# Performance work log

Hardware: AMD Instinct MI355X
Metric: run time of the kernel (lower is better)

Reference implementation:

```python
import jax, jax.numpy as jnp
import numpy as np

N = 50000      # nodes
E = 800000     # edges (avg degree 16)
D_IN, D_H, D_OUT = 128, 128, 64


def setup_inputs() -> dict:
    key = jax.random.key(0)
    ks = jax.random.split(key, 12)
    s = 0.05  # weight init scale
    return {
        "x": jax.random.normal(ks[0], (N, D_IN), jnp.float32),
        "edge_index": jax.random.randint(ks[1], (2, E), 0, N, dtype=jnp.int64),
        "Wl0": jax.random.normal(ks[2], (D_H, D_IN), jnp.float32) * s,
        "bl0": jax.random.normal(ks[3], (D_H,), jnp.float32) * s,
        "Wr0": jax.random.normal(ks[4], (D_H, D_IN), jnp.float32) * s,
        "Wl1": jax.random.normal(ks[5], (D_H, D_H), jnp.float32) * s,
        "bl1": jax.random.normal(ks[6], (D_H,), jnp.float32) * s,
        "Wr1": jax.random.normal(ks[7], (D_H, D_H), jnp.float32) * s,
        "Wl2": jax.random.normal(ks[8], (D_OUT, D_H), jnp.float32) * s,
        "bl2": jax.random.normal(ks[9], (D_OUT,), jnp.float32) * s,
        "Wr2": jax.random.normal(ks[10], (D_OUT, D_H), jnp.float32) * s,
    }


def _sage_layer(h, src, dst, Wl, bl, Wr):
    # mean aggregation over incoming neighbors: out[i] = mean_{j in N(i)} h[j]
    n = h.shape[0]
    agg = jax.ops.segment_sum(h[src], dst, num_segments=n)          # [N, D]
    deg = jax.ops.segment_sum(jnp.ones((src.shape[0],), h.dtype), dst,
                              num_segments=n)                        # [N]
    mean = agg / jnp.maximum(deg, 1.0)[:, None]  # empty rows -> 0, matches torch_sparse
    # lin_l(agg) + lin_r(self); lin_r has no bias in PyG SAGEConv
    return mean @ Wl.T + bl + h @ Wr.T


def reference(x, edge_index, Wl0, bl0, Wr0, Wl1, bl1, Wr1, Wl2, bl2, Wr2):
    src, dst = edge_index[1], edge_index[0]  # adj row = dst, col = src
    h = jax.nn.relu(_sage_layer(x, src, dst, Wl0, bl0, Wr0))
    h = jax.nn.relu(_sage_layer(h, src, dst, Wl1, bl1, Wr1))
    h = _sage_layer(h, src, dst, Wl2, bl2, Wr2)
    return jax.nn.log_softmax(h, axis=1)
```

## Files before the change

kernel.cpp:

```cpp
#include <hip/hip_runtime.h>
#include <hip/hip_bf16.h>


typedef __attribute__((ext_vector_type(8))) short bf16x8;
typedef __attribute__((ext_vector_type(4))) float f32x4;

#define NPB 128
#define BCAP 2560
#define EPB 8192
#define EPT 32
#define CPAD 16

__device__ __forceinline__ unsigned short f2bf(float f) {
    unsigned int u = __builtin_bit_cast(unsigned int, f);
    u += 0x7fffu + ((u >> 16) & 1u);
    return (unsigned short)(u >> 16);
}
__device__ __forceinline__ float bf2f(unsigned int bits16) {
    return __builtin_bit_cast(float, bits16 << 16);
}


__global__ __launch_bounds__(256) void distribute_kernel(const int* __restrict__ dst,
                                                         const int* __restrict__ srcv,
                                                         int* __restrict__ gcnt,
                                                         unsigned int* __restrict__ staging,
                                                         int E, int NBc) {
    __shared__ unsigned int stage[EPB];
    __shared__ int hist[400];
    __shared__ int lstart[400];
    __shared__ int gbase[400];
    __shared__ int scanbuf[256];
    int t = threadIdx.x;
    int e0 = blockIdx.x * EPB;
    unsigned int w[EPT];

    for (int b = t; b < NBc + 1; b += 256) hist[b] = 0;
    __syncthreads();

#pragma unroll
    for (int i = 0; i < EPT; ++i) {
        int e = e0 + i * 256 + t;
        unsigned int word = 0xFFFFFFFFu;
        if (e < E) word = ((unsigned int)dst[e] << 16) | (unsigned int)srcv[e];
        w[i] = word;
        int b = (int)(word >> 23); if (b > NBc) b = NBc;
        atomicAdd(&hist[b], 1);
    }
    __syncthreads();

    int b0 = 2 * t, b1 = 2 * t + 1;
    int h0 = (b0 <= NBc) ? hist[b0] : 0;
    int h1 = (b1 <= NBc) ? hist[b1] : 0;
    int pair = h0 + h1;
    scanbuf[t] = pair;
    __syncthreads();
    for (int off = 1; off < 256; off <<= 1) {
        int v = (t >= off) ? scanbuf[t - off] : 0;
        __syncthreads();
        scanbuf[t] += v;
        __syncthreads();
    }
    int excl = scanbuf[t] - pair;
    if (b0 <= NBc) lstart[b0] = excl;
    if (b1 <= NBc) lstart[b1] = excl + h0;
    __syncthreads();

    for (int b = t; b < NBc; b += 256) {
        int h = hist[b];
        gbase[b] = h ? atomicAdd(&gcnt[b * CPAD], h) : 0;
    }
    for (int b = t; b < NBc + 1; b += 256) hist[b] = lstart[b];
    __syncthreads();

#pragma unroll
    for (int i = 0; i < EPT; ++i) {
        unsigned int word = w[i];
        int b = (int)(word >> 23); if (b > NBc) b = NBc;
        int p = atomicAdd(&hist[b], 1);
        stage[p] = word;
    }
    __syncthreads();

    int total = lstart[NBc];
    for (int i = t; i < total; i += 256) {
        unsigned int word = stage[i];
        int b = (int)(word >> 23);
        int gpos = gbase[b] + (i - lstart[b]);
        staging[(size_t)b * BCAP + gpos] = word;
    }
}


__global__ __launch_bounds__(512) void bucket_scan_kernel(const int* __restrict__ gcnt,
                                                          int* __restrict__ base, int NBc,
                                                          int* __restrict__ rowptr_last) {
    __shared__ int sh[512];
    int t = threadIdx.x;
    int v = (t < NBc) ? gcnt[t * CPAD] : 0;
    sh[t] = v; __syncthreads();
    for (int off = 1; off < 512; off <<= 1) {
        int u = (t >= off) ? sh[t - off] : 0;
        __syncthreads();
        sh[t] += u;
        __syncthreads();
    }
    if (t < NBc) base[t] = sh[t] - v;
    if (t == 511) *rowptr_last = sh[511];
}


__global__ __launch_bounds__(256) void build_kernel(const unsigned int* __restrict__ staging,
                                                    const int* __restrict__ gcnt,
                                                    const int* __restrict__ base,
                                                    int* __restrict__ row_ptr,
                                                    int* __restrict__ adj, int N) {
    __shared__ int hist[NPB];
    __shared__ int scn[NPB];
    int b = blockIdx.x;
    int t = threadIdx.x;
    int n0 = b * NPB;
    int nb = N - n0; if (nb > NPB) nb = NPB;
    int ec = gcnt[b * CPAD];
    int bb = base[b];
    const unsigned int* st = staging + (size_t)b * BCAP;

    if (t < NPB) hist[t] = 0;
    __syncthreads();
    for (int i = t; i < ec; i += 256)
        atomicAdd(&hist[(st[i] >> 16) & (NPB - 1)], 1);
    __syncthreads();

    int v = (t < NPB) ? hist[t] : 0;
    if (t < NPB) scn[t] = v;
    __syncthreads();
    for (int off = 1; off < NPB; off <<= 1) {
        int u = (t >= off && t < NPB) ? scn[t - off] : 0;
        __syncthreads();
        if (t < NPB) scn[t] += u;
        __syncthreads();
    }
    if (t < NPB) hist[t] = scn[t] - v;
    if (t < nb) row_ptr[n0 + t] = bb + (scn[t] - v);
    __syncthreads();

    for (int i = t; i < ec; i += 256) {
        unsigned int pk = st[i];
        int p = atomicAdd(&hist[(pk >> 16) & (NPB - 1)], 1);
        adj[bb + p] = (int)(pk & 0xffffu);
    }
}


__global__ void cast_all_kernel(const float* __restrict__ x,
                                const float* p0, const float* p1, const float* p2,
                                const float* p3, const float* p4, const float* p5,
                                unsigned short* __restrict__ xbf,
                                unsigned short* __restrict__ wbf, int xpairs) {
    int bid = blockIdx.x;
    int xblocks = (xpairs + 255) / 256;
    if (bid < xblocks) {
        int i = bid * 256 + threadIdx.x;
        if (i < xpairs) {
            float2 v = ((const float2*)x)[i];
            unsigned int p = (unsigned int)f2bf(v.x) | ((unsigned int)f2bf(v.y) << 16);
            ((unsigned int*)xbf)[i] = p;
        }
    } else {
        int w = (bid - xblocks) * 256 + threadIdx.x;
        if (w < 40960) {
            const float* src;
            int local;
            if      (w < 8192)  { src = p0; local = w; }
            else if (w < 16384) { src = p1; local = w - 8192; }
            else if (w < 24576) { src = p2; local = w - 16384; }
            else if (w < 32768) { src = p3; local = w - 24576; }
            else if (w < 36864) { src = p4; local = w - 32768; }
            else                { src = p5; local = w - 36864; }
            float2 v = ((const float2*)src)[local];
            unsigned int p = (unsigned int)f2bf(v.x) | ((unsigned int)f2bf(v.y) << 16);
            ((unsigned int*)wbf)[w] = p;
        }
    }
}


__global__ __launch_bounds__(256) void gemm_mfma_kernel(const unsigned short* __restrict__ H,
                                                        const unsigned short* __restrict__ Wl,
                                                        const unsigned short* __restrict__ Wr,
                                                        unsigned short* __restrict__ C,
                                                        int N, int ldC) {
    int wave = threadIdx.x >> 6;
    int lane = threadIdx.x & 63;
    int l15 = lane & 15, quad = lane >> 4;
    int y = blockIdx.y, half = gridDim.y >> 1;
    const unsigned short* W = (y < half) ? Wl : Wr;
    int wrow0 = (y < half ? y : y - half) * 64;
    int col0 = y * 64;
    int m0 = blockIdx.x * 128 + wave * 32;

    int r0 = m0 + l15;      if (r0 > N - 1) r0 = N - 1;
    int r1 = m0 + 16 + l15; if (r1 > N - 1) r1 = N - 1;
    const bf16x8* A0 = (const bf16x8*)(H + (size_t)r0 * 128);
    const bf16x8* A1 = (const bf16x8*)(H + (size_t)r1 * 128);

    f32x4 acc[2][4] = {};
#pragma unroll
    for (int ks = 0; ks < 4; ++ks) {
        int vidx = ks * 4 + quad;
        bf16x8 a0 = A0[vidx];
        bf16x8 a1 = A1[vidx];
#pragma unroll
        for (int j = 0; j < 4; ++j) {
            const bf16x8* B = (const bf16x8*)(W + (size_t)(wrow0 + j * 16 + l15) * 128);
            bf16x8 b = B[vidx];
            acc[0][j] = __builtin_amdgcn_mfma_f32_16x16x32_bf16(a0, b, acc[0][j], 0, 0, 0);
            acc[1][j] = __builtin_amdgcn_mfma_f32_16x16x32_bf16(a1, b, acc[1][j], 0, 0, 0);
        }
    }

#pragma unroll
    for (int i = 0; i < 2; ++i)
#pragma unroll
        for (int j = 0; j < 4; ++j)
#pragma unroll
            for (int r = 0; r < 4; ++r) {
                int row = m0 + i * 16 + quad * 4 + r;
                if (row < N) {
                    int col = col0 + j * 16 + l15;
                    C[(size_t)row * ldC + col] = f2bf(acc[i][j][r]);
                }
            }
}


__global__ __launch_bounds__(256) void agg_relu_kernel(const unsigned short* __restrict__ C,
                                                       const int* __restrict__ row_ptr,
                                                       const int* __restrict__ adj,
                                                       const float* __restrict__ bias,
                                                       unsigned short* __restrict__ hout, int N) {
    int node = (int)((blockIdx.x * blockDim.x + threadIdx.x) >> 6);
    int lane = threadIdx.x & 63;
    if (node >= N) return;
    int beg = row_ptr[node], end = row_ptr[node + 1];
    float sx0 = 0.f, sy0 = 0.f, sx1 = 0.f, sy1 = 0.f;
    float sx2 = 0.f, sy2 = 0.f, sx3 = 0.f, sy3 = 0.f;

    int e = beg;
    while (e < end) {
        int cnt = end - e; if (cnt > 64) cnt = 64;
        int ll = lane; if (ll > cnt - 1) ll = cnt - 1;
        int myidx = adj[e + ll];

        int i = 0;
        for (; i + 8 <= cnt; i += 8) {
            int s0 = __shfl(myidx, i + 0), s1 = __shfl(myidx, i + 1);
            int s2 = __shfl(myidx, i + 2), s3 = __shfl(myidx, i + 3);
            int s4 = __shfl(myidx, i + 4), s5 = __shfl(myidx, i + 5);
            int s6 = __shfl(myidx, i + 6), s7 = __shfl(myidx, i + 7);
            unsigned int v0 = ((const unsigned int*)(C + (size_t)s0 * 256))[lane];
            unsigned int v1 = ((const unsigned int*)(C + (size_t)s1 * 256))[lane];
            unsigned int v2 = ((const unsigned int*)(C + (size_t)s2 * 256))[lane];
            unsigned int v3 = ((const unsigned int*)(C + (size_t)s3 * 256))[lane];
            unsigned int v4 = ((const unsigned int*)(C + (size_t)s4 * 256))[lane];
            unsigned int v5 = ((const unsigned int*)(C + (size_t)s5 * 256))[lane];
            unsigned int v6 = ((const unsigned int*)(C + (size_t)s6 * 256))[lane];
            unsigned int v7 = ((const unsigned int*)(C + (size_t)s7 * 256))[lane];
            sx0 += bf2f(v0 & 0xffffu); sy0 += bf2f(v0 >> 16);
            sx1 += bf2f(v1 & 0xffffu); sy1 += bf2f(v1 >> 16);
            sx2 += bf2f(v2 & 0xffffu); sy2 += bf2f(v2 >> 16);
            sx3 += bf2f(v3 & 0xffffu); sy3 += bf2f(v3 >> 16);
            sx0 += bf2f(v4 & 0xffffu); sy0 += bf2f(v4 >> 16);
            sx1 += bf2f(v5 & 0xffffu); sy1 += bf2f(v5 >> 16);
            sx2 += bf2f(v6 & 0xffffu); sy2 += bf2f(v6 >> 16);
            sx3 += bf2f(v7 & 0xffffu); sy3 += bf2f(v7 >> 16);
        }
        if (i < cnt) {
            int rem = cnt - i, c1 = cnt - 1;
            int t0 = i, t1 = i + 1, t2 = i + 2, t3 = i + 3;
            int t4 = i + 4, t5 = i + 5, t6 = i + 6, t7 = i + 7;
            int s0 = __shfl(myidx, t0 > c1 ? c1 : t0), s1 = __shfl(myidx, t1 > c1 ? c1 : t1);
            int s2 = __shfl(myidx, t2 > c1 ? c1 : t2), s3 = __shfl(myidx, t3 > c1 ? c1 : t3);
            int s4 = __shfl(myidx, t4 > c1 ? c1 : t4), s5 = __shfl(myidx, t5 > c1 ? c1 : t5);
            int s6 = __shfl(myidx, t6 > c1 ? c1 : t6), s7 = __shfl(myidx, t7 > c1 ? c1 : t7);
            unsigned int v0 = ((const unsigned int*)(C + (size_t)s0 * 256))[lane];
            unsigned int v1 = ((const unsigned int*)(C + (size_t)s1 * 256))[lane];
            unsigned int v2 = ((const unsigned int*)(C + (size_t)s2 * 256))[lane];
            unsigned int v3 = ((const unsigned int*)(C + (size_t)s3 * 256))[lane];
            unsigned int v4 = ((const unsigned int*)(C + (size_t)s4 * 256))[lane];
            unsigned int v5 = ((const unsigned int*)(C + (size_t)s5 * 256))[lane];
            unsigned int v6 = ((const unsigned int*)(C + (size_t)s6 * 256))[lane];
            unsigned int v7 = ((const unsigned int*)(C + (size_t)s7 * 256))[lane];
            float m1 = rem > 1 ? 1.f : 0.f, m2 = rem > 2 ? 1.f : 0.f, m3 = rem > 3 ? 1.f : 0.f;
            float m4 = rem > 4 ? 1.f : 0.f, m5 = rem > 5 ? 1.f : 0.f, m6 = rem > 6 ? 1.f : 0.f;
            float m7 = rem > 7 ? 1.f : 0.f;
            sx0 += bf2f(v0 & 0xffffu);      sy0 += bf2f(v0 >> 16);
            sx1 += m1 * bf2f(v1 & 0xffffu); sy1 += m1 * bf2f(v1 >> 16);
            sx2 += m2 * bf2f(v2 & 0xffffu); sy2 += m2 * bf2f(v2 >> 16);
            sx3 += m3 * bf2f(v3 & 0xffffu); sy3 += m3 * bf2f(v3 >> 16);
            sx0 += m4 * bf2f(v4 & 0xffffu); sy0 += m4 * bf2f(v4 >> 16);
            sx1 += m5 * bf2f(v5 & 0xffffu); sy1 += m5 * bf2f(v5 >> 16);
            sx2 += m6 * bf2f(v6 & 0xffffu); sy2 += m6 * bf2f(v6 >> 16);
            sx3 += m7 * bf2f(v7 & 0xffffu); sy3 += m7 * bf2f(v7 >> 16);
        }
        e += cnt;
    }

    float sx = (sx0 + sx1) + (sx2 + sx3);
    float sy = (sy0 + sy1) + (sy2 + sy3);
    int deg = end - beg;
    float inv = 1.0f / (float)(deg > 1 ? deg : 1);
    float2 bb = ((const float2*)bias)[lane];
    unsigned int rv = ((const unsigned int*)(C + (size_t)node * 256))[64 + lane];
    float ox = fmaxf(sx * inv + bb.x + bf2f(rv & 0xffffu), 0.f);
    float oy = fmaxf(sy * inv + bb.y + bf2f(rv >> 16), 0.f);
    unsigned int p = (unsigned int)f2bf(ox) | ((unsigned int)f2bf(oy) << 16);
    ((unsigned int*)(hout + (size_t)node * 128))[lane] = p;
}


__global__ __launch_bounds__(256) void final_kernel(const unsigned short* __restrict__ C,
                                                    const int* __restrict__ row_ptr,
                                                    const int* __restrict__ adj,
                                                    const float* __restrict__ bias,
                                                    float* __restrict__ out, int N) {
    int node = (int)((blockIdx.x * blockDim.x + threadIdx.x) >> 6);
    int lane = threadIdx.x & 63;
    if (node >= N) return;
    int beg = row_ptr[node], end = row_ptr[node + 1];
    float a0 = 0.f, a1 = 0.f, a2 = 0.f, a3 = 0.f;

    int e = beg;
    while (e < end) {
        int cnt = end - e; if (cnt > 64) cnt = 64;
        int ll = lane; if (ll > cnt - 1) ll = cnt - 1;
        int myidx = adj[e + ll];

        int i = 0;
        for (; i + 8 <= cnt; i += 8) {
            int s0 = __shfl(myidx, i + 0), s1 = __shfl(myidx, i + 1);
            int s2 = __shfl(myidx, i + 2), s3 = __shfl(myidx, i + 3);
            int s4 = __shfl(myidx, i + 4), s5 = __shfl(myidx, i + 5);
            int s6 = __shfl(myidx, i + 6), s7 = __shfl(myidx, i + 7);
            float v0 = bf2f((unsigned int)C[(size_t)s0 * 128 + lane]);
            float v1 = bf2f((unsigned int)C[(size_t)s1 * 128 + lane]);
            float v2 = bf2f((unsigned int)C[(size_t)s2 * 128 + lane]);
            float v3 = bf2f((unsigned int)C[(size_t)s3 * 128 + lane]);
            float v4 = bf2f((unsigned int)C[(size_t)s4 * 128 + lane]);
            float v5 = bf2f((unsigned int)C[(size_t)s5 * 128 + lane]);
            float v6 = bf2f((unsigned int)C[(size_t)s6 * 128 + lane]);
            float v7 = bf2f((unsigned int)C[(size_t)s7 * 128 + lane]);
            a0 += v0 + v4; a1 += v1 + v5; a2 += v2 + v6; a3 += v3 + v7;
        }
        if (i < cnt) {
            int rem = cnt - i, c1 = cnt - 1;
            int t;
            t = i + 0; int s0 = __shfl(myidx, t > c1 ? c1 : t);
            t = i + 1; int s1 = __shfl(myidx, t > c1 ? c1 : t);
            t = i + 2; int s2 = __shfl(myidx, t > c1 ? c1 : t);
            t = i + 3; int s3 = __shfl(myidx, t > c1 ? c1 : t);
            t = i + 4; int s4 = __shfl(myidx, t > c1 ? c1 : t);
            t = i + 5; int s5 = __shfl(myidx, t > c1 ? c1 : t);
            t = i + 6; int s6 = __shfl(myidx, t > c1 ? c1 : t);
            t = i + 7; int s7 = __shfl(myidx, t > c1 ? c1 : t);
            float v0 = bf2f((unsigned int)C[(size_t)s0 * 128 + lane]);
            float v1 = bf2f((unsigned int)C[(size_t)s1 * 128 + lane]);
            float v2 = bf2f((unsigned int)C[(size_t)s2 * 128 + lane]);
            float v3 = bf2f((unsigned int)C[(size_t)s3 * 128 + lane]);
            float v4 = bf2f((unsigned int)C[(size_t)s4 * 128 + lane]);
            float v5 = bf2f((unsigned int)C[(size_t)s5 * 128 + lane]);
            float v6 = bf2f((unsigned int)C[(size_t)s6 * 128 + lane]);
            float v7 = bf2f((unsigned int)C[(size_t)s7 * 128 + lane]);
            float m1 = rem > 1 ? 1.f : 0.f, m2 = rem > 2 ? 1.f : 0.f, m3 = rem > 3 ? 1.f : 0.f;
            float m4 = rem > 4 ? 1.f : 0.f, m5 = rem > 5 ? 1.f : 0.f, m6 = rem > 6 ? 1.f : 0.f;
            float m7 = rem > 7 ? 1.f : 0.f;
            a0 += v0 + m4 * v4; a1 += m1 * v1 + m5 * v5;
            a2 += m2 * v2 + m6 * v6; a3 += m3 * v3 + m7 * v7;
        }
        e += cnt;
    }

    float sum = (a0 + a1) + (a2 + a3);
    int deg = end - beg;
    float inv = 1.0f / (float)(deg > 1 ? deg : 1);
    float u = sum * inv + bias[lane] + bf2f((unsigned int)C[(size_t)node * 128 + 64 + lane]);

    float m = u;
#pragma unroll
    for (int off = 32; off > 0; off >>= 1) m = fmaxf(m, __shfl_xor(m, off));
    float ex = __expf(u - m);
    float se = ex;
#pragma unroll
    for (int off = 32; off > 0; off >>= 1) se += __shfl_xor(se, off);
    out[(size_t)node * 64 + lane] = (u - m) - __logf(se);
}


extern "C" void kernel_launch(void* const* d_in, const int* in_sizes, int n_in,
                              void* d_out, int out_size, void* d_ws, size_t ws_size,
                              hipStream_t stream) {
    const float* x   = (const float*)d_in[0];
    const int*   ei  = (const int*)d_in[1];
    const float* Wl0 = (const float*)d_in[2];
    const float* bl0 = (const float*)d_in[3];
    const float* Wr0 = (const float*)d_in[4];
    const float* Wl1 = (const float*)d_in[5];
    const float* bl1 = (const float*)d_in[6];
    const float* Wr1 = (const float*)d_in[7];
    const float* Wl2 = (const float*)d_in[8];
    const float* bl2 = (const float*)d_in[9];
    const float* Wr2 = (const float*)d_in[10];
    float* out = (float*)d_out;

    const int N  = in_sizes[0] / 128;
    const int E  = in_sizes[1] / 2;
    const int NB = (N + NPB - 1) / NPB;

    char* ws = (char*)d_ws;
    auto alloc = [&](size_t bytes) {
        char* p = ws;
        ws += (bytes + 255) & ~(size_t)255;
        return p;
    };
    int*   row_ptr    = (int*)alloc((size_t)(N + 1) * 4);
    int*   adj        = (int*)alloc((size_t)E * 4);
    int*   gcnt       = (int*)alloc((size_t)NB * CPAD * 4);
    int*   bucketBase = (int*)alloc((size_t)NB * 4);
    unsigned int* staging = (unsigned int*)alloc((size_t)NB * BCAP * 4);
    unsigned short* xbf = (unsigned short*)alloc((size_t)N * 128 * 2);
    unsigned short* wbf = (unsigned short*)alloc((size_t)81920 * 2);
    unsigned short* C   = (unsigned short*)alloc((size_t)N * 256 * 2);
    unsigned short* hA  = (unsigned short*)alloc((size_t)N * 128 * 2);
    unsigned short* hB  = (unsigned short*)alloc((size_t)N * 128 * 2);

    const int* dstp = ei;
    const int* srcp = ei + E;

    hipMemsetAsync(gcnt, 0, (size_t)NB * CPAD * 4, stream);
    int distBlocks = (E + EPB - 1) / EPB;
    distribute_kernel<<<distBlocks, 256, 0, stream>>>(dstp, srcp, gcnt, staging, E, NB);
    bucket_scan_kernel<<<1, 512, 0, stream>>>(gcnt, bucketBase, NB, row_ptr + N);
    build_kernel<<<NB, 256, 0, stream>>>(staging, gcnt, bucketBase, row_ptr, adj, N);

    int xpairs = N * 64;
    int castBlocks = (xpairs + 255) / 256 + 160;
    cast_all_kernel<<<castBlocks, 256, 0, stream>>>(x, Wl0, Wr0, Wl1, Wr1, Wl2, Wr2,
                                                    xbf, wbf, xpairs);
    unsigned short* wl0 = wbf;
    unsigned short* wr0 = wbf + 16384;
    unsigned short* wl1 = wbf + 32768;
    unsigned short* wr1 = wbf + 49152;
    unsigned short* wl2 = wbf + 65536;
    unsigned short* wr2 = wbf + 73728;

    dim3 blk(256);
    int gemmRows = (N + 127) / 128;
    int aggBlocks = (N * 64 + 255) / 256;

    gemm_mfma_kernel<<<dim3(gemmRows, 4), blk, 0, stream>>>(xbf, wl0, wr0, C, N, 256);
    agg_relu_kernel<<<aggBlocks, blk, 0, stream>>>(C, row_ptr, adj, bl0, hA, N);
    gemm_mfma_kernel<<<dim3(gemmRows, 4), blk, 0, stream>>>(hA, wl1, wr1, C, N, 256);
    agg_relu_kernel<<<aggBlocks, blk, 0, stream>>>(C, row_ptr, adj, bl1, hB, N);
    gemm_mfma_kernel<<<dim3(gemmRows, 2), blk, 0, stream>>>(hB, wl2, wr2, C, N, 128);
    final_kernel<<<aggBlocks, blk, 0, stream>>>(C, row_ptr, adj, bl2, out, N);
}
```

Baseline: 275.6 us.

## Fuse bucket scan and x cast into consumers, vectorize neighbor gathers

The separate bucket-scan kernel is removed; each build block now computes its own bucket base by summing the preceding bucket counts, and the last block writes row_ptr[N]. The fp32-to-bf16 cast of x is folded into the first GEMM, which reads fp32 rows and packs them in registers, so the xbf intermediate buffer and its pass over memory disappear. The aggregation and final kernels now gather 16-byte bf16x8 chunks, with lane groups each handling a different neighbor, and finish with cross-group shuffle reductions. This cuts launches and gives wider, more parallel gathers. The cost is a redundant prefix sum in every build block, and the first GEMM now reads twice the bytes for its A operand.

```diff
diff --git a/kernel.cpp b/kernel.cpp
--- a/kernel.cpp
+++ b/kernel.cpp
@@ -18,6 +18,14 @@
 }
 __device__ __forceinline__ float bf2f(unsigned int bits16) {
     return __builtin_bit_cast(float, bits16 << 16);
+}
+__device__ __forceinline__ bf16x8 pack8(float4 lo, float4 hi) {
+    bf16x8 r;
+    r[0] = (short)f2bf(lo.x); r[1] = (short)f2bf(lo.y);
+    r[2] = (short)f2bf(lo.z); r[3] = (short)f2bf(lo.w);
+    r[4] = (short)f2bf(hi.x); r[5] = (short)f2bf(hi.y);
+    r[6] = (short)f2bf(hi.z); r[7] = (short)f2bf(hi.w);
+    return r;
 }
 
 
@@ -92,41 +100,29 @@
 }
 
 
-__global__ __launch_bounds__(512) void bucket_scan_kernel(const int* __restrict__ gcnt,
-                                                          int* __restrict__ base, int NBc,
-                                                          int* __restrict__ rowptr_last) {
-    __shared__ int sh[512];
-    int t = threadIdx.x;
-    int v = (t < NBc) ? gcnt[t * CPAD] : 0;
-    sh[t] = v; __syncthreads();
-    for (int off = 1; off < 512; off <<= 1) {
-        int u = (t >= off) ? sh[t - off] : 0;
-        __syncthreads();
-        sh[t] += u;
-        __syncthreads();
-    }
-    if (t < NBc) base[t] = sh[t] - v;
-    if (t == 511) *rowptr_last = sh[511];
-}
-
-
 __global__ __launch_bounds__(256) void build_kernel(const unsigned int* __restrict__ staging,
                                                     const int* __restrict__ gcnt,
-                                                    const int* __restrict__ base,
                                                     int* __restrict__ row_ptr,
-                                                    int* __restrict__ adj, int N) {
+                                                    int* __restrict__ adj, int N, int NBc) {
     __shared__ int hist[NPB];
     __shared__ int scn[NPB];
+    __shared__ int wsum[4];
     int b = blockIdx.x;
     int t = threadIdx.x;
     int n0 = b * NPB;
     int nb = N - n0; if (nb > NPB) nb = NPB;
     int ec = gcnt[b * CPAD];
-    int bb = base[b];
     const unsigned int* st = staging + (size_t)b * BCAP;
 
+    int a = 0;
+    for (int j = t; j < b; j += 256) a += gcnt[j * CPAD];
+#pragma unroll
+    for (int off = 32; off; off >>= 1) a += __shfl_xor(a, off);
+    if ((t & 63) == 0) wsum[t >> 6] = a;
     if (t < NPB) hist[t] = 0;
     __syncthreads();
+    int bb = wsum[0] + wsum[1] + wsum[2] + wsum[3];
+
     for (int i = t; i < ec; i += 256)
         atomicAdd(&hist[(st[i] >> 16) & (NPB - 1)], 1);
     __syncthreads();
@@ -142,6 +138,7 @@
     }
     if (t < NPB) hist[t] = scn[t] - v;
     if (t < nb) row_ptr[n0 + t] = bb + (scn[t] - v);
+    if (b == NBc - 1 && t == 0) row_ptr[N] = bb + ec;
     __syncthreads();
 
     for (int i = t; i < ec; i += 256) {
@@ -152,40 +149,28 @@
 }
 
 
-__global__ void cast_all_kernel(const float* __restrict__ x,
-                                const float* p0, const float* p1, const float* p2,
-                                const float* p3, const float* p4, const float* p5,
-                                unsigned short* __restrict__ xbf,
-                                unsigned short* __restrict__ wbf, int xpairs) {
-    int bid = blockIdx.x;
-    int xblocks = (xpairs + 255) / 256;
-    if (bid < xblocks) {
-        int i = bid * 256 + threadIdx.x;
-        if (i < xpairs) {
-            float2 v = ((const float2*)x)[i];
-            unsigned int p = (unsigned int)f2bf(v.x) | ((unsigned int)f2bf(v.y) << 16);
-            ((unsigned int*)xbf)[i] = p;
-        }
-    } else {
-        int w = (bid - xblocks) * 256 + threadIdx.x;
-        if (w < 40960) {
-            const float* src;
-            int local;
-            if      (w < 8192)  { src = p0; local = w; }
-            else if (w < 16384) { src = p1; local = w - 8192; }
-            else if (w < 24576) { src = p2; local = w - 16384; }
-            else if (w < 32768) { src = p3; local = w - 24576; }
-            else if (w < 36864) { src = p4; local = w - 32768; }
-            else                { src = p5; local = w - 36864; }
-            float2 v = ((const float2*)src)[local];
-            unsigned int p = (unsigned int)f2bf(v.x) | ((unsigned int)f2bf(v.y) << 16);
-            ((unsigned int*)wbf)[w] = p;
-        }
-    }
-}
-
-
-__global__ __launch_bounds__(256) void gemm_mfma_kernel(const unsigned short* __restrict__ H,
+__global__ void cast_w_kernel(const float* p0, const float* p1, const float* p2,
+                              const float* p3, const float* p4, const float* p5,
+                              unsigned short* __restrict__ wbf) {
+    int w = blockIdx.x * 256 + threadIdx.x;
+    if (w < 40960) {
+        const float* src;
+        int local;
+        if      (w < 8192)  { src = p0; local = w; }
+        else if (w < 16384) { src = p1; local = w - 8192; }
+        else if (w < 24576) { src = p2; local = w - 16384; }
+        else if (w < 32768) { src = p3; local = w - 24576; }
+        else if (w < 36864) { src = p4; local = w - 32768; }
+        else                { src = p5; local = w - 36864; }
+        float2 v = ((const float2*)src)[local];
+        unsigned int p = (unsigned int)f2bf(v.x) | ((unsigned int)f2bf(v.y) << 16);
+        ((unsigned int*)wbf)[w] = p;
+    }
+}
+
+
+template<int AF32>
+__global__ __launch_bounds__(256) void gemm_mfma_kernel(const void* __restrict__ Hp,
                                                         const unsigned short* __restrict__ Wl,
                                                         const unsigned short* __restrict__ Wr,
                                                         unsigned short* __restrict__ C,
@@ -201,15 +186,23 @@
 
     int r0 = m0 + l15;      if (r0 > N - 1) r0 = N - 1;
     int r1 = m0 + 16 + l15; if (r1 > N - 1) r1 = N - 1;
-    const bf16x8* A0 = (const bf16x8*)(H + (size_t)r0 * 128);
-    const bf16x8* A1 = (const bf16x8*)(H + (size_t)r1 * 128);
 
     f32x4 acc[2][4] = {};
 #pragma unroll
     for (int ks = 0; ks < 4; ++ks) {
         int vidx = ks * 4 + quad;
-        bf16x8 a0 = A0[vidx];
-        bf16x8 a1 = A1[vidx];
+        bf16x8 a0, a1;
+        if constexpr (AF32) {
+            const float4* A0 = (const float4*)((const float*)Hp + (size_t)r0 * 128);
+            const float4* A1 = (const float4*)((const float*)Hp + (size_t)r1 * 128);
+            a0 = pack8(A0[vidx * 2], A0[vidx * 2 + 1]);
+            a1 = pack8(A1[vidx * 2], A1[vidx * 2 + 1]);
+        } else {
+            const bf16x8* A0 = (const bf16x8*)((const unsigned short*)Hp + (size_t)r0 * 128);
+            const bf16x8* A1 = (const bf16x8*)((const unsigned short*)Hp + (size_t)r1 * 128);
+            a0 = A0[vidx];
+            a1 = A1[vidx];
+        }
 #pragma unroll
         for (int j = 0; j < 4; ++j) {
             const bf16x8* B = (const bf16x8*)(W + (size_t)(wrow0 + j * 16 + l15) * 128);
@@ -242,80 +235,62 @@
     int node = (int)((blockIdx.x * blockDim.x + threadIdx.x) >> 6);
     int lane = threadIdx.x & 63;
     if (node >= N) return;
+    int g = lane >> 4;
+    int c = lane & 15;
     int beg = row_ptr[node], end = row_ptr[node + 1];
-    float sx0 = 0.f, sy0 = 0.f, sx1 = 0.f, sy1 = 0.f;
-    float sx2 = 0.f, sy2 = 0.f, sx3 = 0.f, sy3 = 0.f;
+    float p[8] = {};
 
     int e = beg;
     while (e < end) {
         int cnt = end - e; if (cnt > 64) cnt = 64;
         int ll = lane; if (ll > cnt - 1) ll = cnt - 1;
         int myidx = adj[e + ll];
-
-        int i = 0;
-        for (; i + 8 <= cnt; i += 8) {
-            int s0 = __shfl(myidx, i + 0), s1 = __shfl(myidx, i + 1);
-            int s2 = __shfl(myidx, i + 2), s3 = __shfl(myidx, i + 3);
-            int s4 = __shfl(myidx, i + 4), s5 = __shfl(myidx, i + 5);
-            int s6 = __shfl(myidx, i + 6), s7 = __shfl(myidx, i + 7);
-            unsigned int v0 = ((const unsigned int*)(C + (size_t)s0 * 256))[lane];
-            unsigned int v1 = ((const unsigned int*)(C + (size_t)s1 * 256))[lane];
-            unsigned int v2 = ((const unsigned int*)(C + (size_t)s2 * 256))[lane];
-            unsigned int v3 = ((const unsigned int*)(C + (size_t)s3 * 256))[lane];
-            unsigned int v4 = ((const unsigned int*)(C + (size_t)s4 * 256))[lane];
-            unsigned int v5 = ((const unsigned int*)(C + (size_t)s5 * 256))[lane];
-            unsigned int v6 = ((const unsigned int*)(C + (size_t)s6 * 256))[lane];
-            unsigned int v7 = ((const unsigned int*)(C + (size_t)s7 * 256))[lane];
-            sx0 += bf2f(v0 & 0xffffu); sy0 += bf2f(v0 >> 16);
-            sx1 += bf2f(v1 & 0xffffu); sy1 += bf2f(v1 >> 16);
-            sx2 += bf2f(v2 & 0xffffu); sy2 += bf2f(v2 >> 16);
-            sx3 += bf2f(v3 & 0xffffu); sy3 += bf2f(v3 >> 16);
-            sx0 += bf2f(v4 & 0xffffu); sy0 += bf2f(v4 >> 16);
-            sx1 += bf2f(v5 & 0xffffu); sy1 += bf2f(v5 >> 16);
-            sx2 += bf2f(v6 & 0xffffu); sy2 += bf2f(v6 >> 16);
-            sx3 += bf2f(v7 & 0xffffu); sy3 += bf2f(v7 >> 16);
-        }
-        if (i < cnt) {
-            int rem = cnt - i, c1 = cnt - 1;
-            int t0 = i, t1 = i + 1, t2 = i + 2, t3 = i + 3;
-            int t4 = i + 4, t5 = i + 5, t6 = i + 6, t7 = i + 7;
-            int s0 = __shfl(myidx, t0 > c1 ? c1 : t0), s1 = __shfl(myidx, t1 > c1 ? c1 : t1);
-            int s2 = __shfl(myidx, t2 > c1 ? c1 : t2), s3 = __shfl(myidx, t3 > c1 ? c1 : t3);
-            int s4 = __shfl(myidx, t4 > c1 ? c1 : t4), s5 = __shfl(myidx, t5 > c1 ? c1 : t5);
-            int s6 = __shfl(myidx, t6 > c1 ? c1 : t6), s7 = __shfl(myidx, t7 > c1 ? c1 : t7);
-            unsigned int v0 = ((const unsigned int*)(C + (size_t)s0 * 256))[lane];
-            unsigned int v1 = ((const unsigned int*)(C + (size_t)s1 * 256))[lane];
-            unsigned int v2 = ((const unsigned int*)(C + (size_t)s2 * 256))[lane];
-            unsigned int v3 = ((const unsigned int*)(C + (size_t)s3 * 256))[lane];
-            unsigned int v4 = ((const unsigned int*)(C + (size_t)s4 * 256))[lane];
-            unsigned int v5 = ((const unsigned int*)(C + (size_t)s5 * 256))[lane];
-            unsigned int v6 = ((const unsigned int*)(C + (size_t)s6 * 256))[lane];
-            unsigned int v7 = ((const unsigned int*)(C + (size_t)s7 * 256))[lane];
-            float m1 = rem > 1 ? 1.f : 0.f, m2 = rem > 2 ? 1.f : 0.f, m3 = rem > 3 ? 1.f : 0.f;
-            float m4 = rem > 4 ? 1.f : 0.f, m5 = rem > 5 ? 1.f : 0.f, m6 = rem > 6 ? 1.f : 0.f;
-            float m7 = rem > 7 ? 1.f : 0.f;
-            sx0 += bf2f(v0 & 0xffffu);      sy0 += bf2f(v0 >> 16);
-            sx1 += m1 * bf2f(v1 & 0xffffu); sy1 += m1 * bf2f(v1 >> 16);
-            sx2 += m2 * bf2f(v2 & 0xffffu); sy2 += m2 * bf2f(v2 >> 16);
-            sx3 += m3 * bf2f(v3 & 0xffffu); sy3 += m3 * bf2f(v3 >> 16);
-            sx0 += m4 * bf2f(v4 & 0xffffu); sy0 += m4 * bf2f(v4 >> 16);
-            sx1 += m5 * bf2f(v5 & 0xffffu); sy1 += m5 * bf2f(v5 >> 16);
-            sx2 += m6 * bf2f(v6 & 0xffffu); sy2 += m6 * bf2f(v6 >> 16);
-            sx3 += m7 * bf2f(v7 & 0xffffu); sy3 += m7 * bf2f(v7 >> 16);
+        int c1 = cnt - 1;
+        for (int i = 0; i < cnt; i += 16) {
+            int t0 = i + g, t1 = i + 4 + g, t2 = i + 8 + g, t3 = i + 12 + g;
+            int s0 = __shfl(myidx, t0 > c1 ? c1 : t0);
+            int s1 = __shfl(myidx, t1 > c1 ? c1 : t1);
+            int s2 = __shfl(myidx, t2 > c1 ? c1 : t2);
+            int s3 = __shfl(myidx, t3 > c1 ? c1 : t3);
+            float m0 = t0 < cnt ? 1.f : 0.f;
+            float m1 = t1 < cnt ? 1.f : 0.f;
+            float m2 = t2 < cnt ? 1.f : 0.f;
+            float m3 = t3 < cnt ? 1.f : 0.f;
+            bf16x8 v0 = ((const bf16x8*)(C + (size_t)s0 * 256))[c];
+            bf16x8 v1 = ((const bf16x8*)(C + (size_t)s1 * 256))[c];
+            bf16x8 v2 = ((const bf16x8*)(C + (size_t)s2 * 256))[c];
+            bf16x8 v3 = ((const bf16x8*)(C + (size_t)s3 * 256))[c];
+#pragma unroll
+            for (int k = 0; k < 8; ++k) {
+                p[k] += m0 * bf2f((unsigned short)v0[k]);
+                p[k] += m1 * bf2f((unsigned short)v1[k]);
+                p[k] += m2 * bf2f((unsigned short)v2[k]);
+                p[k] += m3 * bf2f((unsigned short)v3[k]);
+            }
         }
         e += cnt;
     }
 
-    float sx = (sx0 + sx1) + (sx2 + sx3);
-    float sy = (sy0 + sy1) + (sy2 + sy3);
+#pragma unroll
+    for (int k = 0; k < 8; ++k) {
+        p[k] += __shfl_xor(p[k], 16);
+        p[k] += __shfl_xor(p[k], 32);
+    }
+
     int deg = end - beg;
     float inv = 1.0f / (float)(deg > 1 ? deg : 1);
-    float2 bb = ((const float2*)bias)[lane];
-    unsigned int rv = ((const unsigned int*)(C + (size_t)node * 256))[64 + lane];
-    float ox = fmaxf(sx * inv + bb.x + bf2f(rv & 0xffffu), 0.f);
-    float oy = fmaxf(sy * inv + bb.y + bf2f(rv >> 16), 0.f);
-    unsigned int p = (unsigned int)f2bf(ox) | ((unsigned int)f2bf(oy) << 16);
-    ((unsigned int*)(hout + (size_t)node * 128))[lane] = p;
+    bf16x8 sv = ((const bf16x8*)(C + (size_t)node * 256))[16 + c];
+    float4 b0 = ((const float4*)bias)[2 * c];
+    float4 b1 = ((const float4*)bias)[2 * c + 1];
+    float bb[8] = {b0.x, b0.y, b0.z, b0.w, b1.x, b1.y, b1.z, b1.w};
+    bf16x8 o;
+#pragma unroll
+    for (int k = 0; k < 8; ++k) {
+        float v = fmaxf(p[k] * inv + bb[k] + bf2f((unsigned short)sv[k]), 0.f);
+        o[k] = (short)f2bf(v);
+    }
+    if (g == 0)
+        ((bf16x8*)(hout + (size_t)node * 128))[c] = o;
 }
 
 
@@ -327,72 +302,70 @@
     int node = (int)((blockIdx.x * blockDim.x + threadIdx.x) >> 6);
     int lane = threadIdx.x & 63;
     if (node >= N) return;
+    int g = lane >> 3;
+    int c = lane & 7;
     int beg = row_ptr[node], end = row_ptr[node + 1];
-    float a0 = 0.f, a1 = 0.f, a2 = 0.f, a3 = 0.f;
+    float p[8] = {};
 
     int e = beg;
     while (e < end) {
         int cnt = end - e; if (cnt > 64) cnt = 64;
         int ll = lane; if (ll > cnt - 1) ll = cnt - 1;
         int myidx = adj[e + ll];
-
-        int i = 0;
-        for (; i + 8 <= cnt; i += 8) {
-            int s0 = __shfl(myidx, i + 0), s1 = __shfl(myidx, i + 1);
-            int s2 = __shfl(myidx, i + 2), s3 = __shfl(myidx, i + 3);
-            int s4 = __shfl(myidx, i + 4), s5 = __shfl(myidx, i + 5);
-            int s6 = __shfl(myidx, i + 6), s7 = __shfl(myidx, i + 7);
-            float v0 = bf2f((unsigned int)C[(size_t)s0 * 128 + lane]);
-            float v1 = bf2f((unsigned int)C[(size_t)s1 * 128 + lane]);
-            float v2 = bf2f((unsigned int)C[(size_t)s2 * 128 + lane]);
-            float v3 = bf2f((unsigned int)C[(size_t)s3 * 128 + lane]);
-            float v4 = bf2f((unsigned int)C[(size_t)s4 * 128 + lane]);
-            float v5 = bf2f((unsigned int)C[(size_t)s5 * 128 + lane]);
-            float v6 = bf2f((unsigned int)C[(size_t)s6 * 128 + lane]);
-            float v7 = bf2f((unsigned int)C[(size_t)s7 * 128 + lane]);
-            a0 += v0 + v4; a1 += v1 + v5; a2 += v2 + v6; a3 += v3 + v7;
-        }
-        if (i < cnt) {
-            int rem = cnt - i, c1 = cnt - 1;
-            int t;
-            t = i + 0; int s0 = __shfl(myidx, t > c1 ? c1 : t);
-            t = i + 1; int s1 = __shfl(myidx, t > c1 ? c1 : t);
-            t = i + 2; int s2 = __shfl(myidx, t > c1 ? c1 : t);
-            t = i + 3; int s3 = __shfl(myidx, t > c1 ? c1 : t);
-            t = i + 4; int s4 = __shfl(myidx, t > c1 ? c1 : t);
-            t = i + 5; int s5 = __shfl(myidx, t > c1 ? c1 : t);
-            t = i + 6; int s6 = __shfl(myidx, t > c1 ? c1 : t);
-            t = i + 7; int s7 = __shfl(myidx, t > c1 ? c1 : t);
-            float v0 = bf2f((unsigned int)C[(size_t)s0 * 128 + lane]);
-            float v1 = bf2f((unsigned int)C[(size_t)s1 * 128 + lane]);
-            float v2 = bf2f((unsigned int)C[(size_t)s2 * 128 + lane]);
-            float v3 = bf2f((unsigned int)C[(size_t)s3 * 128 + lane]);
-            float v4 = bf2f((unsigned int)C[(size_t)s4 * 128 + lane]);
-            float v5 = bf2f((unsigned int)C[(size_t)s5 * 128 + lane]);
-            float v6 = bf2f((unsigned int)C[(size_t)s6 * 128 + lane]);
-            float v7 = bf2f((unsigned int)C[(size_t)s7 * 128 + lane]);
-            float m1 = rem > 1 ? 1.f : 0.f, m2 = rem > 2 ? 1.f : 0.f, m3 = rem > 3 ? 1.f : 0.f;
-            float m4 = rem > 4 ? 1.f : 0.f, m5 = rem > 5 ? 1.f : 0.f, m6 = rem > 6 ? 1.f : 0.f;
-            float m7 = rem > 7 ? 1.f : 0.f;
-            a0 += v0 + m4 * v4; a1 += m1 * v1 + m5 * v5;
-            a2 += m2 * v2 + m6 * v6; a3 += m3 * v3 + m7 * v7;
+        int c1 = cnt - 1;
+        for (int i = 0; i < cnt; i += 16) {
+            int ta = i + g, tb = i + 8 + g;
+            int sa = __shfl(myidx, ta > c1 ? c1 : ta);
+            int sb = __shfl(myidx, tb > c1 ? c1 : tb);
+            float ma = ta < cnt ? 1.f : 0.f;
+            float mb = tb < cnt ? 1.f : 0.f;
+            bf16x8 va = ((const bf16x8*)(C + (size_t)sa * 128))[c];
+            bf16x8 vb = ((const bf16x8*)(C + (size_t)sb * 128))[c];
+#pragma unroll
+            for (int k = 0; k < 8; ++k) {
+                p[k] += ma * bf2f((unsigned short)va[k]);
+                p[k] += mb * bf2f((unsigned short)vb[k]);
+            }
         }
         e += cnt;
     }
 
-    float sum = (a0 + a1) + (a2 + a3);
+#pragma unroll
+    for (int k = 0; k < 8; ++k) {
+        p[k] += __shfl_xor(p[k], 8);
+        p[k] += __shfl_xor(p[k], 16);
+        p[k] += __shfl_xor(p[k], 32);
+    }
+
     int deg = end - beg;
     float inv = 1.0f / (float)(deg > 1 ? deg : 1);
-    float u = sum * inv + bias[lane] + bf2f((unsigned int)C[(size_t)node * 128 + 64 + lane]);
-
-    float m = u;
-#pragma unroll
-    for (int off = 32; off > 0; off >>= 1) m = fmaxf(m, __shfl_xor(m, off));
-    float ex = __expf(u - m);
-    float se = ex;
-#pragma unroll
-    for (int off = 32; off > 0; off >>= 1) se += __shfl_xor(se, off);
-    out[(size_t)node * 64 + lane] = (u - m) - __logf(se);
+    bf16x8 sv = ((const bf16x8*)(C + (size_t)node * 128))[8 + c];
+    float4 b0 = ((const float4*)bias)[2 * c];
+    float4 b1 = ((const float4*)bias)[2 * c + 1];
+    float bb[8] = {b0.x, b0.y, b0.z, b0.w, b1.x, b1.y, b1.z, b1.w};
+    float u[8];
+#pragma unroll
+    for (int k = 0; k < 8; ++k)
+        u[k] = p[k] * inv + bb[k] + bf2f((unsigned short)sv[k]);
+
+    float m = u[0];
+#pragma unroll
+    for (int k = 1; k < 8; ++k) m = fmaxf(m, u[k]);
+#pragma unroll
+    for (int off = 1; off < 8; off <<= 1) m = fmaxf(m, __shfl_xor(m, off));
+    float se = 0.f;
+#pragma unroll
+    for (int k = 0; k < 8; ++k) se += __expf(u[k] - m);
+#pragma unroll
+    for (int off = 1; off < 8; off <<= 1) se += __shfl_xor(se, off);
+    float ls = __logf(se);
+
+    if (g == 0) {
+        float4 o0 = {u[0] - m - ls, u[1] - m - ls, u[2] - m - ls, u[3] - m - ls};
+        float4 o1 = {u[4] - m - ls, u[5] - m - ls, u[6] - m - ls, u[7] - m - ls};
+        ((float4*)(out + (size_t)node * 64))[2 * c] = o0;
+        ((float4*)(out + (size_t)node * 64))[2 * c + 1] = o1;
+    }
 }
 
 
@@ -425,9 +398,7 @@
     int*   row_ptr    = (int*)alloc((size_t)(N + 1) * 4);
     int*   adj        = (int*)alloc((size_t)E * 4);
     int*   gcnt       = (int*)alloc((size_t)NB * CPAD * 4);
-    int*   bucketBase = (int*)alloc((size_t)NB * 4);
     unsigned int* staging = (unsigned int*)alloc((size_t)NB * BCAP * 4);
-    unsigned short* xbf = (unsigned short*)alloc((size_t)N * 128 * 2);
     unsigned short* wbf = (unsigned short*)alloc((size_t)81920 * 2);
     unsigned short* C   = (unsigned short*)alloc((size_t)N * 256 * 2);
     unsigned short* hA  = (unsigned short*)alloc((size_t)N * 128 * 2);
@@ -439,13 +410,9 @@
     hipMemsetAsync(gcnt, 0, (size_t)NB * CPAD * 4, stream);
     int distBlocks = (E + EPB - 1) / EPB;
     distribute_kernel<<<distBlocks, 256, 0, stream>>>(dstp, srcp, gcnt, staging, E, NB);
-    bucket_scan_kernel<<<1, 512, 0, stream>>>(gcnt, bucketBase, NB, row_ptr + N);
-    build_kernel<<<NB, 256, 0, stream>>>(staging, gcnt, bucketBase, row_ptr, adj, N);
-
-    int xpairs = N * 64;
-    int castBlocks = (xpairs + 255) / 256 + 160;
-    cast_all_kernel<<<castBlocks, 256, 0, stream>>>(x, Wl0, Wr0, Wl1, Wr1, Wl2, Wr2,
-                                                    xbf, wbf, xpairs);
+    build_kernel<<<NB, 256, 0, stream>>>(staging, gcnt, row_ptr, adj, N, NB);
+
+    cast_w_kernel<<<160, 256, 0, stream>>>(Wl0, Wr0, Wl1, Wr1, Wl2, Wr2, wbf);
     unsigned short* wl0 = wbf;
     unsigned short* wr0 = wbf + 16384;
     unsigned short* wl1 = wbf + 32768;
@@ -457,10 +424,10 @@
     int gemmRows = (N + 127) / 128;
     int aggBlocks = (N * 64 + 255) / 256;
 
-    gemm_mfma_kernel<<<dim3(gemmRows, 4), blk, 0, stream>>>(xbf, wl0, wr0, C, N, 256);
+    gemm_mfma_kernel<1><<<dim3(gemmRows, 4), blk, 0, stream>>>((const void*)x, wl0, wr0, C, N, 256);
     agg_relu_kernel<<<aggBlocks, blk, 0, stream>>>(C, row_ptr, adj, bl0, hA, N);
-    gemm_mfma_kernel<<<dim3(gemmRows, 4), blk, 0, stream>>>(hA, wl1, wr1, C, N, 256);
+    gemm_mfma_kernel<0><<<dim3(gemmRows, 4), blk, 0, stream>>>((const void*)hA, wl1, wr1, C, N, 256);
     agg_relu_kernel<<<aggBlocks, blk, 0, stream>>>(C, row_ptr, adj, bl1, hB, N);
-    gemm_mfma_kernel<<<dim3(gemmRows, 2), blk, 0, stream>>>(hB, wl2, wr2, C, N, 128);
+    gemm_mfma_kernel<0><<<dim3(gemmRows, 2), blk, 0, stream>>>((const void*)hB, wl2, wr2, C, N, 128);
     final_kernel<<<aggBlocks, blk, 0, stream>>>(C, row_ptr, adj, bl2, out, N);
 }
```

Measured after the change: 283.0 us. 2.7% more time.
